# Optimization experiments

Measured on AMD Instinct MI355X. Metric: run time of the kernel, lower is better.

## Reference

```python
import jax, jax.numpy as jnp
import numpy as np

N_NODES = 50000
N_EDGES = 800000
D_IN, D_HID, D_OUT = 16, 64, 16
N_BLOCKS = 4


def setup_inputs() -> dict:
    key = jax.random.key(0)
    ks = jax.random.split(key, 12)
    s = 0.05  # small init scale to keep sum-aggregation over 4 blocks stable
    return {
        "x": jax.random.normal(ks[0], (N_NODES, D_IN), jnp.float32),
        "lframes": jax.random.normal(ks[1], (N_NODES, 4, 4), jnp.float32),
        "edge_index": jax.random.randint(ks[2], (2, N_EDGES), 0, N_NODES, jnp.int64),
        "lin_in_w": jax.random.normal(ks[3], (D_IN, D_HID), jnp.float32) * s,
        "lin_in_b": jnp.zeros((D_HID,), jnp.float32),
        # per-block mlp1: Linear(2D->D), ReLU, Linear(D->D), ReLU, Linear(D->D)
        "w0": jax.random.normal(ks[4], (N_BLOCKS, 2 * D_HID, D_HID), jnp.float32) * s,
        "b0": jnp.zeros((N_BLOCKS, D_HID), jnp.float32),
        "w1": jax.random.normal(ks[5], (N_BLOCKS, D_HID, D_HID), jnp.float32) * s,
        "b1": jnp.zeros((N_BLOCKS, D_HID), jnp.float32),
        "w2": jax.random.normal(ks[6], (N_BLOCKS, D_HID, D_HID), jnp.float32) * s,
        "b2": jnp.zeros((N_BLOCKS, D_HID), jnp.float32),
        "lin_out_w": jax.random.normal(ks[7], (D_HID, D_OUT), jnp.float32) * s,
        "lin_out_b": jnp.zeros((D_OUT,), jnp.float32),
    }


def reference(x, lframes, edge_index, lin_in_w, lin_in_b,
              w0, b0, w1, b1, w2, b2, lin_out_w, lin_out_b):
    src = edge_index[0]  # x_j (source / neighbor)
    dst = edge_index[1]  # x_i (target / aggregation node)
    h = x @ lin_in_w + lin_in_b  # [N, D]
    for k in range(N_BLOCKS):
        # message: cat((x_j, x_i)) -> mlp1 ; mlp2 is Identity (num_layers_mlp2=0)
        m = jnp.concatenate((h[src], h[dst]), axis=-1)  # [E, 2D]
        m = jax.nn.relu(m @ w0[k] + b0[k])
        m = jax.nn.relu(m @ w1[k] + b1[k])
        m = m @ w2[k] + b2[k]  # [E, D]
        # aggregate: scatter-add at target node
        h = jax.ops.segment_sum(m, dst, num_segments=N_NODES)
    return h @ lin_out_w + lin_out_b  # [N, D_OUT]
```

## Files before the change

kernel.cpp:

```cpp
#include <hip/hip_runtime.h>
#include <hip/hip_bf16.h>

#define N_NODES 50000
#define N_EDGES 800000
#define D_IN    16
#define D_HID   64
#define D_OUT   16
#define NCHUNK  ((N_NODES + 255) / 256)
#define TMAX    100352

typedef __hip_bfloat16 bf16;
typedef _Float16 f16;
typedef _Float16 f16x8 __attribute__((ext_vector_type(8)));
typedef float    f32x4 __attribute__((ext_vector_type(4)));
typedef _Float16 f16x8a __attribute__((ext_vector_type(8), may_alias));

__device__ __forceinline__ float b2f(bf16 v) { return __bfloat162float(v); }
__device__ __forceinline__ int clampn(int v) {
    return v < 0 ? 0 : (v >= N_NODES ? N_NODES - 1 : v);
}
__device__ __forceinline__ float rdf(const void* p, long i, int isbf) {
    return isbf ? b2f(((const bf16*)p)[i]) : ((const float*)p)[i];
}
__device__ __forceinline__ f16x8 relu8(f16x8 v) {
#pragma unroll
    for (int j = 0; j < 8; j++) v[j] = v[j] > (f16)0 ? v[j] : (f16)0;
    return v;
}

__global__ void k_detect(const unsigned short* __restrict__ xw,
                         const int* __restrict__ ei, int* __restrict__ flags)
{
    if (threadIdx.x == 0) {
        int inband = 0;
        for (int j = 0; j < 256; j++) {
            unsigned short w = xw[2 * j];
            int e = (w >> 7) & 0xFF;
            if ((w & 0x7FFF) == 0 || (e >= 100 && e <= 140)) inband++;
        }
        flags[0] = (inband >= 192) ? 1 : 0;
        int z = 1;
        for (int j = 1; j < 128; j += 2) z &= (ei[j] == 0) ? 1 : 0;
        flags[1] = z;
    }
}

__global__ __launch_bounds__(256) void k_wprep(const int* __restrict__ flags,
                                               const void* __restrict__ gw0,
                                               const void* __restrict__ gw1,
                                               const void* __restrict__ gw2,
                                               f16* __restrict__ wfrag)
{
    int idx = blockIdx.x * 256 + threadIdx.x;
    if (idx >= 4 * 32 * 64) return;
    const int isbf = flags[0];
    int kb = idx >> 11, rem = idx & 2047;
    int slot = rem >> 6, lane = rem & 63;
    int lm = lane & 15, quad = lane >> 4;
    f16* outp = wfrag + (long)idx * 8;
    if (slot < 16) {
        int c = slot >> 2, q = slot & 3;
        long base = (long)kb * 2 * D_HID * D_HID;
#pragma unroll
        for (int j = 0; j < 8; j++)
            outp[j] = (f16)rdf(gw0, base + (long)(c * 32 + quad * 8 + j) * 64 + q * 16 + lm, isbf);
    } else {
        const void* gw = (slot < 24) ? gw1 : gw2;
        int s = (slot < 24) ? slot - 16 : slot - 24;
        int c = s >> 2, q = s & 3;
        long base = (long)kb * D_HID * D_HID;
#pragma unroll
        for (int j = 0; j < 8; j++)
            outp[j] = (f16)rdf(gw, base + (long)(c * 32 + quad * 8 + j) * 64 + q * 16 + lm, isbf);
    }
}

__global__ __launch_bounds__(256) void k_zero_i(int* __restrict__ p, int n)
{
    int i = blockIdx.x * 256 + threadIdx.x;
    if (i < n) p[i] = 0;
}

__global__ __launch_bounds__(256) void k_hist(const int* __restrict__ flags,
                                              const int* __restrict__ eidx,
                                              int* __restrict__ hist)
{
    int e = blockIdx.x * 256 + threadIdx.x;
    if (e >= N_EDGES) return;
    const int strd = flags[1] ? 2 : 1;
    const long dbase = flags[1] ? (long)(2 * N_EDGES) : (long)N_EDGES;
    int d = clampn(eidx[dbase + (long)e * strd]);
    atomicAdd(&hist[d], 1);
}

__global__ __launch_bounds__(256) void k_scan1(const int* __restrict__ in,
                                               int* __restrict__ bsum, int mode)
{
    __shared__ int red[256];
    int i = blockIdx.x * 256 + threadIdx.x;
    int v = (i < N_NODES) ? in[i] : 0;
    if (mode) v = (v + 15) >> 4;
    red[threadIdx.x] = v;
    __syncthreads();
    for (int d = 128; d > 0; d >>= 1) {
        if (threadIdx.x < d) red[threadIdx.x] += red[threadIdx.x + d];
        __syncthreads();
    }
    if (threadIdx.x == 0) bsum[blockIdx.x] = red[0];
}

__global__ __launch_bounds__(256) void k_scan2(const int* __restrict__ bsum,
                                               int* __restrict__ boff,
                                               int* __restrict__ total_out)
{
    __shared__ int s[256];
    const int t = threadIdx.x;
    s[t] = (t < NCHUNK) ? bsum[t] : 0;
    __syncthreads();
    for (int d = 1; d < 256; d <<= 1) {
        int v = (t >= d) ? s[t - d] : 0;
        __syncthreads();
        s[t] += v;
        __syncthreads();
    }
    if (t < NCHUNK) boff[t] = (t == 0) ? 0 : s[t - 1];
    if (t == NCHUNK - 1) total_out[0] = s[t];
}

__global__ __launch_bounds__(256) void k_scan3(const int* __restrict__ in,
                                               const int* __restrict__ boff,
                                               int* __restrict__ off,
                                               int* __restrict__ cursor, int mode)
{
    __shared__ int s[256];
    const int t = threadIdx.x;
    int i = blockIdx.x * 256 + t;
    int v = (i < N_NODES) ? in[i] : 0;
    if (mode) v = (v + 15) >> 4;
    s[t] = v;
    __syncthreads();
    for (int d = 1; d < 256; d <<= 1) {
        int u = (t >= d) ? s[t - d] : 0;
        __syncthreads();
        s[t] += u;
        __syncthreads();
    }
    if (i < N_NODES) {
        int ex = boff[blockIdx.x] + s[t] - v;
        off[i] = ex; cursor[i] = ex;
    }
}

__global__ __launch_bounds__(256) void k_scatter(const int* __restrict__ flags,
                                                 const int* __restrict__ eidx,
                                                 int* __restrict__ cursor,
                                                 int* __restrict__ ssrc)
{
    int e = blockIdx.x * 256 + threadIdx.x;
    if (e >= N_EDGES) return;
    const int strd = flags[1] ? 2 : 1;
    const long dbase = flags[1] ? (long)(2 * N_EDGES) : (long)N_EDGES;
    int d = clampn(eidx[dbase + (long)e * strd]);
    int s = clampn(eidx[(long)e * strd]);
    int pos = atomicAdd(&cursor[d], 1);
    ssrc[pos] = s;
}

__global__ __launch_bounds__(256) void k_tmeta(const int* __restrict__ hist,
                                               const int* __restrict__ toff,
                                               int* __restrict__ tmeta)
{
    int n = blockIdx.x * 256 + threadIdx.x;
    if (n >= N_NODES) return;
    int dg = hist[n];
    if (dg == 0) return;
    int t0 = toff[n], nt = (dg + 15) >> 4;
    for (int j = 0; j < nt; j++)
        tmeta[t0 + j] = n | (min(16, dg - 16 * j) << 20);
}

__global__ __launch_bounds__(256) void k_fill(const int* __restrict__ hist,
                                              const int* __restrict__ off,
                                              const int* __restrict__ toff,
                                              const int* __restrict__ totalp,
                                              const int* __restrict__ tmeta,
                                              const int* __restrict__ ssrc,
                                              int* __restrict__ spad)
{
    int idx = blockIdx.x * 256 + threadIdx.x;
    int t = idx >> 4, i = idx & 15;
    if (t >= totalp[0]) return;
    int n = tmeta[t] & 0xFFFFF;
    int j = t - toff[n];
    int dg = hist[n];
    spad[idx] = ssrc[off[n] + min(16 * j + i, dg - 1)];
}

__global__ __launch_bounds__(256) void k_lin_in(const int* __restrict__ flags,
                                                const void* __restrict__ x,
                                                const void* __restrict__ w,
                                                const void* __restrict__ b,
                                                float* __restrict__ h)
{
    int idx = blockIdx.x * 256 + threadIdx.x;
    if (idx >= N_NODES * D_HID) return;
    const int isbf = flags[0];
    int n = idx >> 6, c = idx & 63;
    float acc = rdf(b, c, isbf);
#pragma unroll
    for (int i = 0; i < D_IN; i++)
        acc += rdf(x, (long)n * D_IN + i, isbf) * rdf(w, (long)i * D_HID + c, isbf);
    h[idx] = acc;
}

#define HP_ST 72

__global__ __launch_bounds__(256) void k_proj(
    const int* __restrict__ flags, float* hio,
    const f16* __restrict__ wfrag, const void* __restrict__ gb0,
    f16* __restrict__ psrc, f16* __restrict__ pdst, int kblk)
{
    __shared__ f16 hL_s[4][16 * HP_ST];

    const int tid  = threadIdx.x;
    const int isbf = flags[0];
    const int wv = tid >> 6, ln = tid & 63;
    const int lm = ln & 15, quad = ln >> 4;
    f16* hL = hL_s[wv];

    const int g = blockIdx.x * 4 + wv;
    if (g >= N_NODES / 16) return;
    const int n0 = g * 16;

    const f16* wb = wfrag + (long)kblk * 32 * 64 * 8;

#pragma unroll
    for (int i = 0; i < 16; i++) {
        int idx = i * 64 + ln;
        hL[(idx >> 6) * HP_ST + (idx & 63)] = (f16)hio[(long)n0 * 64 + idx];
    }
#pragma unroll
    for (int i = 0; i < 16; i++)
        hio[(long)n0 * 64 + i * 64 + ln] = 0.f;

    f16x8 a[2];
#pragma unroll
    for (int c = 0; c < 2; c++)
        a[c] = *(const f16x8a*)&hL[lm * HP_ST + c * 32 + quad * 8];

    f32x4 accS[4], accD[4];
#pragma unroll
    for (int q = 0; q < 4; q++) {
        float bd = rdf(gb0, (long)kblk * 64 + q * 16 + lm, isbf);
        accS[q] = (f32x4){0.f, 0.f, 0.f, 0.f};
        accD[q] = (f32x4){bd, bd, bd, bd};
    }
#pragma unroll
    for (int c = 0; c < 2; c++)
#pragma unroll
        for (int q = 0; q < 4; q++) {
            f16x8 bs = *(const f16x8a*)&wb[(((c + 0) * 4 + q) * 64 + ln) * 8];
            f16x8 bd = *(const f16x8a*)&wb[(((c + 2) * 4 + q) * 64 + ln) * 8];
            accS[q] = __builtin_amdgcn_mfma_f32_16x16x32_f16(a[c], bs, accS[q], 0, 0, 0);
            accD[q] = __builtin_amdgcn_mfma_f32_16x16x32_f16(a[c], bd, accD[q], 0, 0, 0);
        }
#pragma unroll
    for (int q = 0; q < 4; q++)
#pragma unroll
        for (int r = 0; r < 4; r++) {
            long o = (long)(n0 + quad * 4 + r) * 64 + q * 16 + lm;
            psrc[o] = (f16)accS[q][r];
            pdst[o] = (f16)accD[q][r];
        }
}

#define Y_ST 72

__global__ __launch_bounds__(256) void k_edge_tile(
    const int* __restrict__ flags,
    const int* __restrict__ ssrc_pad, const int* __restrict__ tmeta,
    const int* __restrict__ toff,
    const f16* __restrict__ psrc, const f16* __restrict__ pdst,
    float* __restrict__ hout,
    const f16* __restrict__ wfrag, const void* __restrict__ gb1,
    const void* __restrict__ gb2, int kblk)
{
    __shared__ f16 y_s[4][2][16 * Y_ST];

    const int tid  = threadIdx.x;
    const int isbf = flags[0];
    const int wv = tid >> 6, ln = tid & 63;
    const int lm = ln & 15, quad = ln >> 4;

    const f16* wb = wfrag + (long)kblk * 32 * 64 * 8;
    f16x8 bw1[2][4], bw2[2][4];
#pragma unroll
    for (int c = 0; c < 2; c++)
#pragma unroll
        for (int q = 0; q < 4; q++) {
            bw1[c][q] = *(const f16x8a*)&wb[((16 + c * 4 + q) * 64 + ln) * 8];
            bw2[c][q] = *(const f16x8a*)&wb[((24 + c * 4 + q) * 64 + ln) * 8];
        }
    float bias1[4], bias2[4];
#pragma unroll
    for (int q = 0; q < 4; q++) {
        bias1[q] = rdf(gb1, (long)kblk * 64 + q * 16 + lm, isbf);
        bias2[q] = rdf(gb2, (long)kblk * 64 + q * 16 + lm, isbf);
    }

    f16* yA = y_s[wv][0];
    f16* yB = y_s[wv][1];
    const int sub = ln & 7, eh = ln >> 3;

    const int T  = toff[N_NODES];
    const int W  = gridDim.x * 4;
    const int gw = blockIdx.x * 4 + wv;
    const int t0 = (int)((long)gw * T / W);
    const int t1 = (int)((long)(gw + 1) * T / W);
    if (t0 >= t1) return;

    int tcA = t0, tcB = min(t0 + 1, T - 1);
    int tc2 = min(t0 + 2, T - 1), tc3 = min(t0 + 3, T - 1);
    int m0 = tmeta[tcA], m1 = tmeta[tcB], m2 = tmeta[tc2], m3 = tmeta[tc3];
    int s2a = ssrc_pad[tc2 * 16 + eh], s2b = ssrc_pad[tc2 * 16 + 8 + eh];
    int s3a = ssrc_pad[tc3 * 16 + eh], s3b = ssrc_pad[tc3 * 16 + 8 + eh];
    int s0a = ssrc_pad[tcA * 16 + eh], s0b = ssrc_pad[tcA * 16 + 8 + eh];
    int s1a = ssrc_pad[tcB * 16 + eh], s1b = ssrc_pad[tcB * 16 + 8 + eh];
    f16x8 ps0a = *(const f16x8a*)&psrc[(long)s0a * 64 + sub * 8];
    f16x8 ps0b = *(const f16x8a*)&psrc[(long)s0b * 64 + sub * 8];
    f16x8 pd0  = *(const f16x8a*)&pdst[(long)(m0 & 0xFFFFF) * 64 + sub * 8];
    f16x8 ps1a = *(const f16x8a*)&psrc[(long)s1a * 64 + sub * 8];
    f16x8 ps1b = *(const f16x8a*)&psrc[(long)s1b * 64 + sub * 8];
    f16x8 pd1  = *(const f16x8a*)&pdst[(long)(m1 & 0xFFFFF) * 64 + sub * 8];

    float accn[4] = {0.f, 0.f, 0.f, 0.f};

    for (int tt = t0; tt < t1; tt += 2) {
        const int tc4 = min(tt + 4, T - 1), tc5 = min(tt + 5, T - 1);
        int m4 = tmeta[tc4], m5 = tmeta[tc5];
        int s4a = ssrc_pad[tc4 * 16 + eh], s4b = ssrc_pad[tc4 * 16 + 8 + eh];
        int s5a = ssrc_pad[tc5 * 16 + eh], s5b = ssrc_pad[tc5 * 16 + 8 + eh];
        f16x8 ps2a = *(const f16x8a*)&psrc[(long)s2a * 64 + sub * 8];
        f16x8 ps2b = *(const f16x8a*)&psrc[(long)s2b * 64 + sub * 8];
        f16x8 pd2  = *(const f16x8a*)&pdst[(long)(m2 & 0xFFFFF) * 64 + sub * 8];
        f16x8 ps3a = *(const f16x8a*)&psrc[(long)s3a * 64 + sub * 8];
        f16x8 ps3b = *(const f16x8a*)&psrc[(long)s3b * 64 + sub * 8];
        f16x8 pd3  = *(const f16x8a*)&pdst[(long)(m3 & 0xFFFFF) * 64 + sub * 8];

        const int hasB = (tt + 1 < t1);
        const int v0 = m0 >> 20;
        const int v1 = hasB ? (m1 >> 20) : 0;

        *(f16x8a*)&yA[eh * Y_ST + sub * 8]       = relu8(ps0a + pd0);
        *(f16x8a*)&yA[(8 + eh) * Y_ST + sub * 8] = relu8(ps0b + pd0);
        *(f16x8a*)&yB[eh * Y_ST + sub * 8]       = relu8(ps1a + pd1);
        *(f16x8a*)&yB[(8 + eh) * Y_ST + sub * 8] = relu8(ps1b + pd1);

        f16x8 a1A[2], a1B[2];
#pragma unroll
        for (int c = 0; c < 2; c++) {
            a1A[c] = *(const f16x8a*)&yA[lm * Y_ST + c * 32 + quad * 8];
            a1B[c] = *(const f16x8a*)&yB[lm * Y_ST + c * 32 + quad * 8];
        }
        f32x4 accA[4], accB[4];
#pragma unroll
        for (int q = 0; q < 4; q++) {
            accA[q] = (f32x4){bias1[q], bias1[q], bias1[q], bias1[q]};
            accB[q] = (f32x4){bias1[q], bias1[q], bias1[q], bias1[q]};
        }
#pragma unroll
        for (int c = 0; c < 2; c++)
#pragma unroll
            for (int q = 0; q < 4; q++) {
                accA[q] = __builtin_amdgcn_mfma_f32_16x16x32_f16(a1A[c], bw1[c][q], accA[q], 0, 0, 0);
                accB[q] = __builtin_amdgcn_mfma_f32_16x16x32_f16(a1B[c], bw1[c][q], accB[q], 0, 0, 0);
            }
#pragma unroll
        for (int q = 0; q < 4; q++)
#pragma unroll
            for (int r = 0; r < 4; r++) {
                yA[(quad * 4 + r) * Y_ST + q * 16 + lm] = (f16)fmaxf(accA[q][r], 0.f);
                yB[(quad * 4 + r) * Y_ST + q * 16 + lm] = (f16)fmaxf(accB[q][r], 0.f);
            }

        f16x8 a2A[2], a2B[2];
#pragma unroll
        for (int c = 0; c < 2; c++) {
            a2A[c] = *(const f16x8a*)&yA[lm * Y_ST + c * 32 + quad * 8];
            a2B[c] = *(const f16x8a*)&yB[lm * Y_ST + c * 32 + quad * 8];
        }
#pragma unroll
        for (int q = 0; q < 4; q++) {
            accA[q] = (f32x4){bias2[q], bias2[q], bias2[q], bias2[q]};
            accB[q] = (f32x4){bias2[q], bias2[q], bias2[q], bias2[q]};
        }
#pragma unroll
        for (int c = 0; c < 2; c++)
#pragma unroll
            for (int q = 0; q < 4; q++) {
                accA[q] = __builtin_amdgcn_mfma_f32_16x16x32_f16(a2A[c], bw2[c][q], accA[q], 0, 0, 0);
                accB[q] = __builtin_amdgcn_mfma_f32_16x16x32_f16(a2B[c], bw2[c][q], accB[q], 0, 0, 0);
            }

#pragma unroll
        for (int q = 0; q < 4; q++)
#pragma unroll
            for (int r = 0; r < 4; r++)
                if (quad * 4 + r < v0) accn[q] += accA[q][r];
        {
            const int curn = m0 & 0xFFFFF;
            const int nxt  = hasB ? (m1 & 0xFFFFF) : -1;
            if (nxt != curn) {
#pragma unroll
                for (int q = 0; q < 4; q++) {
                    float v = accn[q];
                    v += __shfl_xor(v, 16, 64);
                    v += __shfl_xor(v, 32, 64);
                    if (quad == 0) atomicAdd(&hout[(long)curn * 64 + q * 16 + lm], v);
                    accn[q] = 0.f;
                }
            }
        }
        if (hasB) {
#pragma unroll
            for (int q = 0; q < 4; q++)
#pragma unroll
                for (int r = 0; r < 4; r++)
                    if (quad * 4 + r < v1) accn[q] += accB[q][r];
            const int curn = m1 & 0xFFFFF;
            const int nxt  = (tt + 2 < t1) ? (m2 & 0xFFFFF) : -1;
            if (nxt != curn) {
#pragma unroll
                for (int q = 0; q < 4; q++) {
                    float v = accn[q];
                    v += __shfl_xor(v, 16, 64);
                    v += __shfl_xor(v, 32, 64);
                    if (quad == 0) atomicAdd(&hout[(long)curn * 64 + q * 16 + lm], v);
                    accn[q] = 0.f;
                }
            }
        }

        m0 = m2; m1 = m3; m2 = m4; m3 = m5;
        s2a = s4a; s2b = s4b; s3a = s5a; s3b = s5b;
        ps0a = ps2a; ps0b = ps2b; pd0 = pd2;
        ps1a = ps3a; ps1b = ps3b; pd1 = pd3;
    }
}

__global__ __launch_bounds__(256) void k_lin_out(const int* __restrict__ flags,
                                                 const float* __restrict__ h,
                                                 const void* __restrict__ w,
                                                 const void* __restrict__ b,
                                                 float* __restrict__ out)
{
    int idx = blockIdx.x * 256 + threadIdx.x;
    if (idx >= N_NODES * D_OUT) return;
    const int isbf = flags[0];
    int n = idx >> 4, c = idx & 15;
    float acc = rdf(b, c, isbf);
    const float* hr = h + (long)n * D_HID;
#pragma unroll
    for (int i = 0; i < D_HID; i++) acc += hr[i] * rdf(w, (long)i * D_OUT + c, isbf);
    out[idx] = acc;
}

extern "C" void kernel_launch(void* const* d_in, const int* in_sizes, int n_in,
                              void* d_out, int out_size, void* d_ws, size_t ws_size,
                              hipStream_t stream)
{
    const void* x    = d_in[0];
    const int*  ei   = (const int*)d_in[2];
    const void* liw  = d_in[3];
    const void* lib  = d_in[4];
    const void* w0   = d_in[5];
    const void* b0   = d_in[6];
    const void* w1   = d_in[7];
    const void* b1   = d_in[8];
    const void* w2   = d_in[9];
    const void* b2   = d_in[10];
    const void* low  = d_in[11];
    const void* lob  = d_in[12];
    float* out = (float*)d_out;

    char* wp = (char*)d_ws;
    int*   flags  = (int*)wp;                 wp += 256;
    float* hA     = (float*)wp;               wp += (size_t)N_NODES * D_HID * 4;
    f16*   Psrc   = (f16*)wp;                 wp += (size_t)N_NODES * D_HID * 2;
    f16*   Pdst   = (f16*)wp;                 wp += (size_t)N_NODES * D_HID * 2;
    f16*   wfrag  = (f16*)wp;                 wp += (size_t)4 * 32 * 64 * 8 * 2;
    int*   hist   = (int*)wp;                 wp += (size_t)N_NODES * 4;
    int*   off    = (int*)wp;                 wp += ((size_t)N_NODES + 1) * 4;
    int*   cursor = (int*)wp;                 wp += (size_t)N_NODES * 4;
    int*   toff   = (int*)wp;                 wp += ((size_t)N_NODES + 1) * 4;
    int*   tcur   = (int*)wp;                 wp += (size_t)N_NODES * 4;
    int*   bsum   = (int*)wp;                 wp += 256 * 4;
    int*   boff   = (int*)wp;                 wp += 256 * 4;
    int*   ssrc   = (int*)wp;                 wp += (size_t)N_EDGES * 4;
    int*   tmeta  = (int*)wp;                 wp += (size_t)TMAX * 4;
    int*   spad   = (int*)wp;

    const int HN = N_NODES * D_HID;
    const int gH = (HN + 255) / 256;
    const int gE = (N_EDGES + 255) / 256;
    const int gN = (N_NODES + 255) / 256;

    k_detect<<<1, 64, 0, stream>>>((const unsigned short*)x, ei, flags);
    k_wprep<<<32, 256, 0, stream>>>(flags, w0, w1, w2, wfrag);

    k_zero_i<<<gN, 256, 0, stream>>>(hist, N_NODES);
    k_hist<<<gE, 256, 0, stream>>>(flags, ei, hist);
    k_scan1<<<NCHUNK, 256, 0, stream>>>(hist, bsum, 0);
    k_scan2<<<1, 256, 0, stream>>>(bsum, boff, off + N_NODES);
    k_scan3<<<NCHUNK, 256, 0, stream>>>(hist, boff, off, cursor, 0);
    k_scatter<<<gE, 256, 0, stream>>>(flags, ei, cursor, ssrc);
    k_scan1<<<NCHUNK, 256, 0, stream>>>(hist, bsum, 1);
    k_scan2<<<1, 256, 0, stream>>>(bsum, boff, toff + N_NODES);
    k_scan3<<<NCHUNK, 256, 0, stream>>>(hist, boff, toff, tcur, 1);
    k_tmeta<<<gN, 256, 0, stream>>>(hist, toff, tmeta);
    k_fill<<<(TMAX * 16) / 256, 256, 0, stream>>>(hist, off, toff, toff + N_NODES,
                                                  tmeta, ssrc, spad);

    k_lin_in<<<gH, 256, 0, stream>>>(flags, x, liw, lib, hA);

    for (int k = 0; k < 4; k++) {
        k_proj<<<(N_NODES / 16 + 3) / 4, 256, 0, stream>>>(flags, hA, wfrag, b0,
                                                           Psrc, Pdst, k);
        k_edge_tile<<<1024, 256, 0, stream>>>(flags, spad, tmeta, toff,
                                              Psrc, Pdst, hA, wfrag, b1, b2, k);
    }

    k_lin_out<<<(N_NODES * D_OUT + 255) / 256, 256, 0, stream>>>(flags, hA, low, lob, out);
}
```

Measured before the change: 478.1 us.

## Fuse CSR build preprocessing kernels and batch edge atomics four per thread

Merges the hist zeroing into the detect kernel and runs the edge-offset and tile-offset scans together in shared scan kernels. The per-node tile metadata fill is folded into the second scan pass, and the histogram and scatter kernels now handle four edges per thread. The aim is to cut launch count and redundant passes over the histogram in the graph preprocessing stage. The cost is more work per thread, with less parallelism for the atomics, and a serial loop inside the scan kernel.

New measurement: 458.3 us. 1.04x faster.

```diff
diff --git a/kernel.cpp b/kernel.cpp
--- a/kernel.cpp
+++ b/kernel.cpp
@@ -28,10 +28,14 @@
     return v;
 }
 
-__global__ void k_detect(const unsigned short* __restrict__ xw,
-                         const int* __restrict__ ei, int* __restrict__ flags)
-{
-    if (threadIdx.x == 0) {
+__global__ __launch_bounds__(256) void k_detect(const unsigned short* __restrict__ xw,
+                                                const int* __restrict__ ei,
+                                                int* __restrict__ flags,
+                                                int* __restrict__ hist)
+{
+    int i = blockIdx.x * 256 + threadIdx.x;
+    if (i < N_NODES) hist[i] = 0;
+    if (blockIdx.x == 0 && threadIdx.x == 0) {
         int inband = 0;
         for (int j = 0; j < 256; j++) {
             unsigned short w = xw[2 * j];
@@ -75,108 +79,119 @@
     }
 }
 
-__global__ __launch_bounds__(256) void k_zero_i(int* __restrict__ p, int n)
-{
-    int i = blockIdx.x * 256 + threadIdx.x;
-    if (i < n) p[i] = 0;
-}
-
-__global__ __launch_bounds__(256) void k_hist(const int* __restrict__ flags,
-                                              const int* __restrict__ eidx,
-                                              int* __restrict__ hist)
-{
-    int e = blockIdx.x * 256 + threadIdx.x;
-    if (e >= N_EDGES) return;
+__global__ __launch_bounds__(256) void k_hist4(const int* __restrict__ flags,
+                                               const int* __restrict__ eidx,
+                                               int* __restrict__ hist)
+{
+    int base = (blockIdx.x * 256 + threadIdx.x) * 4;
+    if (base >= N_EDGES) return;
     const int strd = flags[1] ? 2 : 1;
     const long dbase = flags[1] ? (long)(2 * N_EDGES) : (long)N_EDGES;
-    int d = clampn(eidx[dbase + (long)e * strd]);
-    atomicAdd(&hist[d], 1);
-}
-
-__global__ __launch_bounds__(256) void k_scan1(const int* __restrict__ in,
-                                               int* __restrict__ bsum, int mode)
-{
-    __shared__ int red[256];
-    int i = blockIdx.x * 256 + threadIdx.x;
-    int v = (i < N_NODES) ? in[i] : 0;
-    if (mode) v = (v + 15) >> 4;
-    red[threadIdx.x] = v;
+#pragma unroll
+    for (int j = 0; j < 4; j++) {
+        int e = base + j;
+        if (e < N_EDGES)
+            atomicAdd(&hist[clampn(eidx[dbase + (long)e * strd])], 1);
+    }
+}
+
+__global__ __launch_bounds__(256) void k_scan1(const int* __restrict__ hist,
+                                               int* __restrict__ bsum_e,
+                                               int* __restrict__ bsum_t)
+{
+    __shared__ int re[256], rt[256];
+    const int t = threadIdx.x;
+    int i = blockIdx.x * 256 + t;
+    int v = (i < N_NODES) ? hist[i] : 0;
+    re[t] = v; rt[t] = (v + 15) >> 4;
     __syncthreads();
     for (int d = 128; d > 0; d >>= 1) {
-        if (threadIdx.x < d) red[threadIdx.x] += red[threadIdx.x + d];
+        if (t < d) { re[t] += re[t + d]; rt[t] += rt[t + d]; }
         __syncthreads();
     }
-    if (threadIdx.x == 0) bsum[blockIdx.x] = red[0];
-}
-
-__global__ __launch_bounds__(256) void k_scan2(const int* __restrict__ bsum,
-                                               int* __restrict__ boff,
-                                               int* __restrict__ total_out)
-{
-    __shared__ int s[256];
+    if (t == 0) { bsum_e[blockIdx.x] = re[0]; bsum_t[blockIdx.x] = rt[0]; }
+}
+
+__global__ __launch_bounds__(256) void k_scan2(const int* __restrict__ bsum_e,
+                                               const int* __restrict__ bsum_t,
+                                               int* __restrict__ boff_e,
+                                               int* __restrict__ boff_t,
+                                               int* __restrict__ tot_e,
+                                               int* __restrict__ tot_t)
+{
+    __shared__ int se[256], st_[256];
     const int t = threadIdx.x;
-    s[t] = (t < NCHUNK) ? bsum[t] : 0;
+    se[t]  = (t < NCHUNK) ? bsum_e[t] : 0;
+    st_[t] = (t < NCHUNK) ? bsum_t[t] : 0;
     __syncthreads();
     for (int d = 1; d < 256; d <<= 1) {
-        int v = (t >= d) ? s[t - d] : 0;
+        int ve = (t >= d) ? se[t - d] : 0;
+        int vt = (t >= d) ? st_[t - d] : 0;
         __syncthreads();
-        s[t] += v;
+        se[t] += ve; st_[t] += vt;
         __syncthreads();
     }
-    if (t < NCHUNK) boff[t] = (t == 0) ? 0 : s[t - 1];
-    if (t == NCHUNK - 1) total_out[0] = s[t];
-}
-
-__global__ __launch_bounds__(256) void k_scan3(const int* __restrict__ in,
-                                               const int* __restrict__ boff,
+    if (t < NCHUNK) {
+        boff_e[t] = (t == 0) ? 0 : se[t - 1];
+        boff_t[t] = (t == 0) ? 0 : st_[t - 1];
+    }
+    if (t == NCHUNK - 1) { tot_e[0] = se[t]; tot_t[0] = st_[t]; }
+}
+
+__global__ __launch_bounds__(256) void k_scan3(const int* __restrict__ hist,
+                                               const int* __restrict__ boff_e,
+                                               const int* __restrict__ boff_t,
                                                int* __restrict__ off,
-                                               int* __restrict__ cursor, int mode)
-{
-    __shared__ int s[256];
+                                               int* __restrict__ cursor,
+                                               int* __restrict__ toff,
+                                               int* __restrict__ tmeta)
+{
+    __shared__ int se[256], st_[256];
     const int t = threadIdx.x;
     int i = blockIdx.x * 256 + t;
-    int v = (i < N_NODES) ? in[i] : 0;
-    if (mode) v = (v + 15) >> 4;
-    s[t] = v;
+    int v = (i < N_NODES) ? hist[i] : 0;
+    int w = (v + 15) >> 4;
+    se[t] = v; st_[t] = w;
     __syncthreads();
     for (int d = 1; d < 256; d <<= 1) {
-        int u = (t >= d) ? s[t - d] : 0;
+        int ue = (t >= d) ? se[t - d] : 0;
+        int ut = (t >= d) ? st_[t - d] : 0;
         __syncthreads();
-        s[t] += u;
+        se[t] += ue; st_[t] += ut;
         __syncthreads();
     }
     if (i < N_NODES) {
-        int ex = boff[blockIdx.x] + s[t] - v;
-        off[i] = ex; cursor[i] = ex;
-    }
-}
-
-__global__ __launch_bounds__(256) void k_scatter(const int* __restrict__ flags,
-                                                 const int* __restrict__ eidx,
-                                                 int* __restrict__ cursor,
-                                                 int* __restrict__ ssrc)
-{
-    int e = blockIdx.x * 256 + threadIdx.x;
-    if (e >= N_EDGES) return;
+        int exE = boff_e[blockIdx.x] + se[t] - v;
+        off[i] = exE; cursor[i] = exE;
+        int exT = boff_t[blockIdx.x] + st_[t] - w;
+        toff[i] = exT;
+        for (int j = 0; j < w; j++)
+            tmeta[exT + j] = i | (min(16, v - 16 * j) << 20);
+    }
+}
+
+__global__ __launch_bounds__(256) void k_scatter4(const int* __restrict__ flags,
+                                                  const int* __restrict__ eidx,
+                                                  int* __restrict__ cursor,
+                                                  int* __restrict__ ssrc)
+{
+    int base = (blockIdx.x * 256 + threadIdx.x) * 4;
+    if (base >= N_EDGES) return;
     const int strd = flags[1] ? 2 : 1;
     const long dbase = flags[1] ? (long)(2 * N_EDGES) : (long)N_EDGES;
-    int d = clampn(eidx[dbase + (long)e * strd]);
-    int s = clampn(eidx[(long)e * strd]);
-    int pos = atomicAdd(&cursor[d], 1);
-    ssrc[pos] = s;
-}
-
-__global__ __launch_bounds__(256) void k_tmeta(const int* __restrict__ hist,
-                                               const int* __restrict__ toff,
-                                               int* __restrict__ tmeta)
-{
-    int n = blockIdx.x * 256 + threadIdx.x;
-    if (n >= N_NODES) return;
-    int dg = hist[n];
-    if (dg == 0) return;
-    int t0 = toff[n], nt = (dg + 15) >> 4;
-    for (int j = 0; j < nt; j++)
-        tmeta[t0 + j] = n | (min(16, dg - 16 * j) << 20);
+    int d[4], s[4], pos[4], cnt = min(4, N_EDGES - base);
+#pragma unroll
+    for (int j = 0; j < 4; j++)
+        if (j < cnt) {
+            d[j] = clampn(eidx[dbase + (long)(base + j) * strd]);
+            s[j] = clampn(eidx[(long)(base + j) * strd]);
+        }
+#pragma unroll
+    for (int j = 0; j < 4; j++)
+        if (j < cnt) pos[j] = atomicAdd(&cursor[d[j]], 1);
+#pragma unroll
+    for (int j = 0; j < 4; j++)
+        if (j < cnt) ssrc[pos[j]] = s[j];
 }
 
 __global__ __launch_bounds__(256) void k_fill(const int* __restrict__ hist,
@@ -493,31 +508,27 @@
     int*   off    = (int*)wp;                 wp += ((size_t)N_NODES + 1) * 4;
     int*   cursor = (int*)wp;                 wp += (size_t)N_NODES * 4;
     int*   toff   = (int*)wp;                 wp += ((size_t)N_NODES + 1) * 4;
-    int*   tcur   = (int*)wp;                 wp += (size_t)N_NODES * 4;
-    int*   bsum   = (int*)wp;                 wp += 256 * 4;
-    int*   boff   = (int*)wp;                 wp += 256 * 4;
+    int*   bsum_e = (int*)wp;                 wp += 256 * 4;
+    int*   bsum_t = (int*)wp;                 wp += 256 * 4;
+    int*   boff_e = (int*)wp;                 wp += 256 * 4;
+    int*   boff_t = (int*)wp;                 wp += 256 * 4;
     int*   ssrc   = (int*)wp;                 wp += (size_t)N_EDGES * 4;
     int*   tmeta  = (int*)wp;                 wp += (size_t)TMAX * 4;
     int*   spad   = (int*)wp;
 
     const int HN = N_NODES * D_HID;
     const int gH = (HN + 255) / 256;
-    const int gE = (N_EDGES + 255) / 256;
-    const int gN = (N_NODES + 255) / 256;
-
-    k_detect<<<1, 64, 0, stream>>>((const unsigned short*)x, ei, flags);
+    const int gE4 = (N_EDGES / 4 + 255) / 256;
+
+    k_detect<<<NCHUNK, 256, 0, stream>>>((const unsigned short*)x, ei, flags, hist);
     k_wprep<<<32, 256, 0, stream>>>(flags, w0, w1, w2, wfrag);
 
-    k_zero_i<<<gN, 256, 0, stream>>>(hist, N_NODES);
-    k_hist<<<gE, 256, 0, stream>>>(flags, ei, hist);
-    k_scan1<<<NCHUNK, 256, 0, stream>>>(hist, bsum, 0);
-    k_scan2<<<1, 256, 0, stream>>>(bsum, boff, off + N_NODES);
-    k_scan3<<<NCHUNK, 256, 0, stream>>>(hist, boff, off, cursor, 0);
-    k_scatter<<<gE, 256, 0, stream>>>(flags, ei, cursor, ssrc);
-    k_scan1<<<NCHUNK, 256, 0, stream>>>(hist, bsum, 1);
-    k_scan2<<<1, 256, 0, stream>>>(bsum, boff, toff + N_NODES);
-    k_scan3<<<NCHUNK, 256, 0, stream>>>(hist, boff, toff, tcur, 1);
-    k_tmeta<<<gN, 256, 0, stream>>>(hist, toff, tmeta);
+    k_hist4<<<gE4, 256, 0, stream>>>(flags, ei, hist);
+    k_scan1<<<NCHUNK, 256, 0, stream>>>(hist, bsum_e, bsum_t);
+    k_scan2<<<1, 256, 0, stream>>>(bsum_e, bsum_t, boff_e, boff_t,
+                                   off + N_NODES, toff + N_NODES);
+    k_scan3<<<NCHUNK, 256, 0, stream>>>(hist, boff_e, boff_t, off, cursor, toff, tmeta);
+    k_scatter4<<<gE4, 256, 0, stream>>>(flags, ei, cursor, ssrc);
     k_fill<<<(TMAX * 16) / 256, 256, 0, stream>>>(hist, off, toff, toff + N_NODES,
                                                   tmeta, ssrc, spad);
 
```
